# Optimization experiments

Measured on AMD Instinct MI355X. Metric: run time of the kernel, lower is better.

Reference implementation:

```python
import jax, jax.numpy as jnp
import numpy as np
from jax import lax

KERNEL = 512

def squash(x, axis=-1):
    sn = jnp.sum(x * x, axis=axis, keepdims=True)
    scale = sn / (1.0 + sn)
    return scale * x / jnp.sqrt(sn + 1e-8)

def setup_inputs() -> dict:
    key = jax.random.key(0)
    ks = jax.random.split(key, 6)
    x = jax.random.normal(ks[0], (4096, 1, 1008), dtype=jnp.float32)
    a = jax.random.uniform(ks[1], (128, 1, 1), dtype=jnp.float32) * 5.0 + 0.1
    w = jax.random.uniform(ks[2], (128, 1, 1), dtype=jnp.float32) * 150.0 + 1.0
    conv_w = jax.random.normal(ks[3], (256, 128, 16), dtype=jnp.float32) * 0.02
    conv_b = jnp.zeros((256,), dtype=jnp.float32)
    W_caps = jax.random.normal(ks[4], (288, 4, 16, 8), dtype=jnp.float32) * 0.01
    return {"x": x, "a": a, "w": w, "conv_w": conv_w, "conv_b": conv_b, "W_caps": W_caps}

def reference(x, a, w, conv_w, conv_b, W_caps):
    # --- WavConv1d: generate wavelet weights on the fly ---
    t = jnp.linspace(-1.0, 1.0, KERNEL, dtype=jnp.float32).reshape(1, 1, KERNEL)
    a_safe = jnp.clip(a, 1e-5, None)
    t_scaled = t / a_safe
    wav_w = jnp.cos(w * t) * jnp.exp(-0.5 * t_scaled ** 2)  # [128,1,512]
    h = lax.conv_general_dilated(x, wav_w, window_strides=(16,), padding='VALID',
                                 dimension_numbers=('NCH', 'OIH', 'NCH'))  # [B,128,32]
    # --- PrimaryCaps1d ---
    p = lax.conv_general_dilated(h, conv_w, window_strides=(2,), padding='VALID',
                                 dimension_numbers=('NCH', 'OIH', 'NCH'))  # [B,256,9]
    p = p + conv_b[None, :, None]
    B = p.shape[0]
    u = squash(p.reshape(B, -1, 8))  # [B,288,8]
    # --- ClassCaps with dynamic routing ---
    # u_hat[b,c,d,o] = sum_i W_caps[c,d,o,i] * u[b,c,i]
    u_hat = jnp.einsum('cdoi,bci->bcdo', W_caps, u)  # [B,288,4,16]
    b_ij = jnp.zeros((B, u_hat.shape[1], u_hat.shape[2], 1), dtype=u_hat.dtype)
    num_routing = 3
    for i in range(num_routing):
        c_ij = jax.nn.softmax(b_ij, axis=2)                      # [B,288,4,1]
        s_j = jnp.sum(c_ij * u_hat, axis=1, keepdims=True)       # [B,1,4,16]
        v_j = squash(s_j, axis=-1)                               # [B,1,4,16]
        if i < num_routing - 1:
            agreement = jnp.sum(u_hat * v_j, axis=-1, keepdims=True)
            b_ij = b_ij + agreement
    v = jnp.squeeze(v_j, axis=1)          # [B,4,16]
    probs = jnp.linalg.norm(v, axis=-1)   # [B,4]
    return probs, jnp.squeeze(c_ij, axis=-1)  # [B,4], [B,288,4]
```

## Files before the change

### kernel.cpp

```cpp
#include <hip/hip_runtime.h>
#include <hip/hip_bf16.h>
#include <math.h>

typedef __attribute__((ext_vector_type(4))) short short4v;
typedef __attribute__((ext_vector_type(8))) short short8;
typedef __attribute__((ext_vector_type(4))) float f32x4;
typedef __attribute__((ext_vector_type(2))) float f32x2;
typedef _Float16 half8 __attribute__((ext_vector_type(8)));

#define BATCH   4096
#define XLEN    1008
#define NOC1    128
#define NPOS    32
#define NOC2    256
#define NQ      9
#define NCAPS   288
#define NDIM    8

#define BWH_OFF   0
#define BPH_OFF   131072
#define H2_OFF    1179648
#define U_OFF     34734080

static __device__ __forceinline__ short f2h(float v) {
    _Float16 h = (_Float16)v;
    return *reinterpret_cast<short*>(&h);
}

static __device__ __forceinline__ f32x2 pkfma(float a, f32x2 b, f32x2 c) {
    f32x2 av = {a, a};
    return av * b + c;
}

template <int CTRL>
static __device__ __forceinline__ float dpp_addf(float x) {
    int y = __builtin_amdgcn_update_dpp(0, __builtin_bit_cast(int, x),
                                        CTRL, 0xf, 0xf, true);
    return x + __builtin_bit_cast(float, y);
}
static __device__ __forceinline__ float rowsum16(float x) {
    x = dpp_addf<0xB1>(x);
    x = dpp_addf<0x4E>(x);
    x = dpp_addf<0x141>(x);
    x = dpp_addf<0x140>(x);
    return x;
}

__global__ __launch_bounds__(256) void k_pack(const float* __restrict__ a,
                                              const float* __restrict__ w,
                                              const float* __restrict__ cw,
                                              short* __restrict__ bwh,
                                              short* __restrict__ bph) {
    int bid = blockIdx.x;
    int tid = threadIdx.x;
    if (bid < 256) {
        int idx = bid * 256 + tid;
        int e    = idx & 7;
        int lane = (idx >> 3) & 63;
        int s    = (idx >> 9) & 15;
        int nt   = idx >> 13;
        int oc = nt * 16 + (lane & 15);
        int k  = s * 32 + (lane >> 4) * 8 + e;
        float t  = -1.0f + 2.0f * (float)k / 511.0f;
        float av = fmaxf(a[oc], 1e-5f);
        float ts = t / av;
        bwh[idx] = f2h(cosf(w[oc] * t) * expf(-0.5f * ts * ts));
    } else {
        int o = (bid - 256) * 256 + tid;
        int e    = o & 7;
        int lane = (o >> 3) & 63;
        int s    = (o >> 9) & 63;
        int nt   = o >> 15;
        int n  = nt * 16 + (lane & 15);
        int j  = lane >> 4;
        int kk = s >> 2;
        int ic = (s & 3) * 32 + j * 8 + e;
        bph[o] = f2h(cw[(n * NOC1 + ic) * 16 + kk]);
    }
}

__global__ __launch_bounds__(256, 2) void k_wavconv_mfma(
        const float* __restrict__ x,
        const short* __restrict__ bwh,
        short* __restrict__ h2) {
    __shared__ short xl[8][1512];

    int tid = threadIdx.x;
    int b0  = blockIdx.x * 8;

    for (int i4 = tid; i4 < 2016; i4 += 256) {
        int b  = i4 / 252;
        int e4 = i4 - b * 252;
        float4 v = *(const float4*)(x + (size_t)(b0 + b) * XLEN + e4 * 4);
        int i    = e4 * 4;
        int slot = i + 8 * (i >> 4);
        short4v hv;
        hv.x = f2h(v.x); hv.y = f2h(v.y); hv.z = f2h(v.z); hv.w = f2h(v.w);
        *(short4v*)&xl[b][slot] = hv;
    }
    __syncthreads();

    int lane = tid & 63;
    int w    = tid >> 6;
    int col  = lane & 15;
    int rg   = lane >> 4;

    f32x4 acc[4][8];
    f32x4 z = {0.f, 0.f, 0.f, 0.f};
#pragma unroll
    for (int tl = 0; tl < 4; ++tl)
#pragma unroll
        for (int nt = 0; nt < 8; ++nt) acc[tl][nt] = z;

    for (int s = 0; s < 16; ++s) {
        half8 Bh[8];
#pragma unroll
        for (int nt = 0; nt < 8; ++nt) {
            size_t off = ((size_t)(nt * 16 + s) * 64 + lane) * 8;
            Bh[nt] = __builtin_bit_cast(half8, *(const short8*)(bwh + off));
        }
#pragma unroll
        for (int tl = 0; tl < 4; ++tl) {
            int mt  = 4 * w + tl;
            int bl  = mt >> 1;
            int pos = (mt & 1) * 16 + col;
            int i    = (pos + 2 * s) * 16 + rg * 8;
            int slot = i + 8 * (i >> 4);
            half8 ah = __builtin_bit_cast(half8, *(const short8*)&xl[bl][slot]);
#pragma unroll
            for (int nt = 0; nt < 8; ++nt)
                acc[tl][nt] = __builtin_amdgcn_mfma_f32_16x16x32_f16(ah, Bh[nt], acc[tl][nt], 0, 0, 0);
        }
    }

#pragma unroll
    for (int tl = 0; tl < 4; ++tl) {
        int mt = 4 * w + tl;
        int b  = b0 + (mt >> 1);
        int ph = (mt & 1) * 16;
#pragma unroll
        for (int nt = 0; nt < 8; ++nt) {
            int oc = nt * 16 + col;
#pragma unroll
            for (int r = 0; r < 4; ++r) {
                int pos = ph + rg * 4 + r;
                h2[((size_t)b * NPOS + pos) * NOC1 + oc] = f2h(acc[tl][nt][r]);
            }
        }
    }
}

__global__ __launch_bounds__(512, 4) void k_conv_mfma(const short* __restrict__ h2,
                                                      const short* __restrict__ bph,
                                                      const float* __restrict__ cb,
                                                      float* __restrict__ u) {
    __shared__ char smem[36864];
    short* A0 = (short*)smem;
    short* A1 = (short*)(smem + 6400);
    float* p_lds = (float*)smem;

    int tid  = threadIdx.x;
    int w    = tid >> 6;
    int lane = tid & 63;
    int col  = lane & 15;
    int rg   = lane >> 4;
    int b0   = blockIdx.x * 8;

    f32x4 acc[5][2];
    f32x4 z = {0.f, 0.f, 0.f, 0.f};
#pragma unroll
    for (int mt = 0; mt < 5; ++mt) { acc[mt][0] = z; acc[mt][1] = z; }

    auto stageA = [&](int s, short* dst) {
        int kk  = s >> 2;
        int icb = (s & 3) * 32;
        if (tid < 288) {
            int m = tid >> 2;
            int g = tid & 3;
            const short* src = h2 +
                ((size_t)(b0 + (m & 7)) * NPOS + (2 * (m >> 3) + kk)) * NOC1 + icb + g * 8;
            *(short8*)&dst[m * 40 + g * 8] = *(const short8*)src;
        }
    };

    auto mfmaStep = [&](int s, const short* A) {
        short8 arow[5];
#pragma unroll
        for (int mt = 0; mt < 5; ++mt)
            arow[mt] = *(const short8*)&A[(mt * 16 + col) * 40 + rg * 8];
#pragma unroll
        for (int n = 0; n < 2; ++n) {
            size_t bo = ((size_t)((w + n * 8) * 64 + s) * 64 + lane) * 8;
            half8 Bh = __builtin_bit_cast(half8, *(const short8*)(bph + bo));
#pragma unroll
            for (int mt = 0; mt < 5; ++mt)
                acc[mt][n] = __builtin_amdgcn_mfma_f32_16x16x32_f16(
                    __builtin_bit_cast(half8, arow[mt]), Bh, acc[mt][n], 0, 0, 0);
        }
    };

    stageA(0, A0);
    __syncthreads();
    for (int s = 0; s < 64; s += 2) {
        if (s + 1 < 64) stageA(s + 1, A1);
        mfmaStep(s, A0);
        __syncthreads();
        if (s + 2 < 64) stageA(s + 2, A0);
        mfmaStep(s + 1, A1);
        __syncthreads();
    }

    int oc2l = w * 16 + col;
    for (int n = 0; n < 2; ++n) {
        float bias = cb[n * 128 + oc2l];
#pragma unroll
        for (int mt = 0; mt < 5; ++mt)
#pragma unroll
            for (int r = 0; r < 4; ++r) {
                int m = mt * 16 + rg * 4 + r;
                if (m < 72)
                    p_lds[(m & 7) * 1152 + oc2l * 9 + (m >> 3)] = acc[mt][n][r] + bias;
            }
        __syncthreads();
        for (int idx = tid; idx < 1152; idx += 512) {
            int lb = idx / 144;
            int cl = idx - lb * 144;
            float* ppt = &p_lds[lb * 1152 + cl * 8];
            float sn = 0.f;
#pragma unroll
            for (int i = 0; i < NDIM; ++i) sn = fmaf(ppt[i], ppt[i], sn);
            float sc = sn / (1.f + sn) / sqrtf(sn + 1e-8f);
            float* ug = u + ((size_t)(b0 + lb) * (NCAPS * NDIM) + (n * 144 + cl) * 8);
            float4 u0 = make_float4(ppt[0] * sc, ppt[1] * sc, ppt[2] * sc, ppt[3] * sc);
            float4 u1 = make_float4(ppt[4] * sc, ppt[5] * sc, ppt[6] * sc, ppt[7] * sc);
            ((float4*)ug)[0] = u0;
            ((float4*)ug)[1] = u1;
        }
        __syncthreads();
    }
}

__global__ __launch_bounds__(512, 4) void k_routing(const float* __restrict__ u,
                                                    const float* __restrict__ Wc,
                                                    float* __restrict__ out) {
    __shared__ float b_lds[2][NCAPS * 4];
    __shared__ float c_lds[2][NCAPS * 4];
    __shared__ float part_lds[2][512];
    __shared__ float v_lds[2][64];

    int tid = threadIdx.x;
    int b0  = blockIdx.x * 2;

    int g = tid >> 6;
    int l = tid & 63;
    int d = l >> 4;
    int o = l & 15;
    int gu = __builtin_amdgcn_readfirstlane(g);

    const float* ub0 = u + (size_t)(b0 + 0) * (NCAPS * NDIM) + gu * 36 * NDIM;
    const float* ub1 = u + (size_t)(b0 + 1) * (NCAPS * NDIM) + gu * 36 * NDIM;

    f32x2 uh[36];
#pragma unroll
    for (int c = 0; c < 36; ++c) {
        int cap = gu * 36 + c;
        const float4* W4 = (const float4*)(Wc + ((size_t)cap * 512) + l * 8);
        float4 A  = W4[0];
        float4 Bv = W4[1];
        f32x2 u0 = {ub0[c * 8 + 0], ub1[c * 8 + 0]};
        f32x2 u1 = {ub0[c * 8 + 1], ub1[c * 8 + 1]};
        f32x2 u2 = {ub0[c * 8 + 2], ub1[c * 8 + 2]};
        f32x2 u3 = {ub0[c * 8 + 3], ub1[c * 8 + 3]};
        f32x2 u4 = {ub0[c * 8 + 4], ub1[c * 8 + 4]};
        f32x2 u5 = {ub0[c * 8 + 5], ub1[c * 8 + 5]};
        f32x2 u6 = {ub0[c * 8 + 6], ub1[c * 8 + 6]};
        f32x2 u7 = {ub0[c * 8 + 7], ub1[c * 8 + 7]};
        f32x2 t = (f32x2){A.x, A.x} * u0;
        t = pkfma(A.y,  u1, t);
        t = pkfma(A.z,  u2, t);
        t = pkfma(A.w,  u3, t);
        t = pkfma(Bv.x, u4, t);
        t = pkfma(Bv.y, u5, t);
        t = pkfma(Bv.z, u6, t);
        t = pkfma(Bv.w, u7, t);
        uh[c] = t;
    }

    for (int r = 0; r < 3; ++r) {
        if (r > 0) {
            __builtin_amdgcn_wave_barrier();
            for (int i = l; i < 72; i += 64) {
                int bb = (i >= 36) ? 1 : 0;
                int cl = i - bb * 36;
                int c  = gu * 36 + cl;
                float4 bv = *(const float4*)&b_lds[bb][c * 4];
                float m  = fmaxf(fmaxf(bv.x, bv.y), fmaxf(bv.z, bv.w));
                float e0 = expf(bv.x - m), e1 = expf(bv.y - m);
                float e2 = expf(bv.z - m), e3 = expf(bv.w - m);
                float inv = 1.f / (e0 + e1 + e2 + e3);
                e0 *= inv; e1 *= inv; e2 *= inv; e3 *= inv;
                *(float4*)&c_lds[bb][c * 4] = make_float4(e0, e1, e2, e3);
                if (r == 2) {
                    *(float4*)(out + 16384 + ((size_t)(b0 + bb) * NCAPS + c) * 4) =
                        make_float4(e0, e1, e2, e3);
                }
            }
            __builtin_amdgcn_wave_barrier();
        }

        f32x2 p = {0.f, 0.f};
        if (r == 0) {
#pragma unroll
            for (int c = 0; c < 36; ++c)
                p = pkfma(0.25f, uh[c], p);
        } else {
#pragma unroll
            for (int c = 0; c < 36; ++c) {
                f32x2 c2 = {c_lds[0][(g * 36 + c) * 4 + d],
                            c_lds[1][(g * 36 + c) * 4 + d]};
                p = c2 * uh[c] + p;
            }
        }
        part_lds[0][tid] = p.x;
        part_lds[1][tid] = p.y;
        __syncthreads();

        if (tid < 128) {
            int bb = tid >> 6;
            int ll = tid & 63;
            float sv = 0.f;
#pragma unroll
            for (int k = 0; k < 8; ++k) sv += part_lds[bb][ll + 64 * k];
            float sq = rowsum16(sv * sv);
            float sc = sq / (1.f + sq) / sqrtf(sq + 1e-8f);
            float v  = sv * sc;
            v_lds[bb][ll] = v;
            if (r == 2) {
                float vv = rowsum16(v * v);
                if ((ll & 15) == 0)
                    out[(size_t)(b0 + bb) * 4 + (ll >> 4)] = sqrtf(vv);
            }
        }
        __syncthreads();

        if (r < 2) {
            f32x2 v01 = {v_lds[0][l], v_lds[1][l]};
#pragma unroll
            for (int c = 0; c < 36; ++c) {
                f32x2 t2 = uh[c] * v01;
                float t0 = rowsum16(t2.x);
                float t1 = rowsum16(t2.y);
                if (o == 0) {
                    if (r == 0) {
                        b_lds[0][(g * 36 + c) * 4 + d] = t0;
                        b_lds[1][(g * 36 + c) * 4 + d] = t1;
                    } else {
                        b_lds[0][(g * 36 + c) * 4 + d] += t0;
                        b_lds[1][(g * 36 + c) * 4 + d] += t1;
                    }
                }
            }
        }
    }
}

extern "C" void kernel_launch(void* const* d_in, const int* in_sizes, int n_in,
                              void* d_out, int out_size, void* d_ws, size_t ws_size,
                              hipStream_t stream) {
    const float* x      = (const float*)d_in[0];
    const float* a      = (const float*)d_in[1];
    const float* w      = (const float*)d_in[2];
    const float* conv_w = (const float*)d_in[3];
    const float* conv_b = (const float*)d_in[4];
    const float* W_caps = (const float*)d_in[5];
    float* out = (float*)d_out;
    char* ws   = (char*)d_ws;

    short*  bwh = (short*)(ws + BWH_OFF);
    short*  bph = (short*)(ws + BPH_OFF);
    short*  h2  = (short*)(ws + H2_OFF);
    float*  u   = (float*)(ws + U_OFF);

    k_pack<<<2304, 256, 0, stream>>>(a, w, conv_w, bwh, bph);
    k_wavconv_mfma<<<BATCH / 8, 256, 0, stream>>>(x, bwh, h2);
    k_conv_mfma<<<BATCH / 8, 512, 0, stream>>>(h2, bph, conv_b, u);
    k_routing<<<BATCH / 2, 512, 0, stream>>>(u, W_caps, out);
}
```

Before: 238.1 us.

## Process four batch items per routing block with 16 waves and 18 capsules each

The routing kernel now runs 1024-thread blocks that each handle four batch items instead of two. Each wave owns 18 capsules instead of 36 and keeps predictions for two item pairs in registers. Every W_caps load is therefore reused across four items, and each thread does half as many capsule iterations per item pair. In exchange the blocks are larger, the cross-wave reduction doubles to 16 partials, and the LDS footprint grows, which may reduce occupancy.

```diff
diff --git a/kernel.cpp b/kernel.cpp
--- a/kernel.cpp
+++ b/kernel.cpp
@@ -240,16 +240,16 @@
     }
 }
 
-__global__ __launch_bounds__(512, 4) void k_routing(const float* __restrict__ u,
-                                                    const float* __restrict__ Wc,
-                                                    float* __restrict__ out) {
-    __shared__ float b_lds[2][NCAPS * 4];
-    __shared__ float c_lds[2][NCAPS * 4];
-    __shared__ float part_lds[2][512];
-    __shared__ float v_lds[2][64];
+__global__ __launch_bounds__(1024, 4) void k_routing(const float* __restrict__ u,
+                                                     const float* __restrict__ Wc,
+                                                     float* __restrict__ out) {
+    __shared__ float b_lds[4][NCAPS * 4];
+    __shared__ float c_lds[4][NCAPS * 4];
+    __shared__ float part_lds[4][1024];
+    __shared__ float v_lds[4][64];
 
     int tid = threadIdx.x;
-    int b0  = blockIdx.x * 2;
+    int b0  = blockIdx.x * 4;
 
     int g = tid >> 6;
     int l = tid & 63;
@@ -257,42 +257,45 @@
     int o = l & 15;
     int gu = __builtin_amdgcn_readfirstlane(g);
 
-    const float* ub0 = u + (size_t)(b0 + 0) * (NCAPS * NDIM) + gu * 36 * NDIM;
-    const float* ub1 = u + (size_t)(b0 + 1) * (NCAPS * NDIM) + gu * 36 * NDIM;
-
-    f32x2 uh[36];
-#pragma unroll
-    for (int c = 0; c < 36; ++c) {
-        int cap = gu * 36 + c;
+    const float* ub0 = u + (size_t)(b0 + 0) * (NCAPS * NDIM) + gu * 18 * NDIM;
+    const float* ub1 = u + (size_t)(b0 + 1) * (NCAPS * NDIM) + gu * 18 * NDIM;
+    const float* ub2 = u + (size_t)(b0 + 2) * (NCAPS * NDIM) + gu * 18 * NDIM;
+    const float* ub3 = u + (size_t)(b0 + 3) * (NCAPS * NDIM) + gu * 18 * NDIM;
+
+    f32x2 uhA[18], uhB[18];
+#pragma unroll
+    for (int c = 0; c < 18; ++c) {
+        int cap = gu * 18 + c;
         const float4* W4 = (const float4*)(Wc + ((size_t)cap * 512) + l * 8);
         float4 A  = W4[0];
         float4 Bv = W4[1];
-        f32x2 u0 = {ub0[c * 8 + 0], ub1[c * 8 + 0]};
-        f32x2 u1 = {ub0[c * 8 + 1], ub1[c * 8 + 1]};
-        f32x2 u2 = {ub0[c * 8 + 2], ub1[c * 8 + 2]};
-        f32x2 u3 = {ub0[c * 8 + 3], ub1[c * 8 + 3]};
-        f32x2 u4 = {ub0[c * 8 + 4], ub1[c * 8 + 4]};
-        f32x2 u5 = {ub0[c * 8 + 5], ub1[c * 8 + 5]};
-        f32x2 u6 = {ub0[c * 8 + 6], ub1[c * 8 + 6]};
-        f32x2 u7 = {ub0[c * 8 + 7], ub1[c * 8 + 7]};
-        f32x2 t = (f32x2){A.x, A.x} * u0;
-        t = pkfma(A.y,  u1, t);
-        t = pkfma(A.z,  u2, t);
-        t = pkfma(A.w,  u3, t);
-        t = pkfma(Bv.x, u4, t);
-        t = pkfma(Bv.y, u5, t);
-        t = pkfma(Bv.z, u6, t);
-        t = pkfma(Bv.w, u7, t);
-        uh[c] = t;
+        f32x2 tA = (f32x2){A.x, A.x} * (f32x2){ub0[c * 8 + 0], ub1[c * 8 + 0]};
+        tA = pkfma(A.y,  (f32x2){ub0[c * 8 + 1], ub1[c * 8 + 1]}, tA);
+        tA = pkfma(A.z,  (f32x2){ub0[c * 8 + 2], ub1[c * 8 + 2]}, tA);
+        tA = pkfma(A.w,  (f32x2){ub0[c * 8 + 3], ub1[c * 8 + 3]}, tA);
+        tA = pkfma(Bv.x, (f32x2){ub0[c * 8 + 4], ub1[c * 8 + 4]}, tA);
+        tA = pkfma(Bv.y, (f32x2){ub0[c * 8 + 5], ub1[c * 8 + 5]}, tA);
+        tA = pkfma(Bv.z, (f32x2){ub0[c * 8 + 6], ub1[c * 8 + 6]}, tA);
+        tA = pkfma(Bv.w, (f32x2){ub0[c * 8 + 7], ub1[c * 8 + 7]}, tA);
+        uhA[c] = tA;
+        f32x2 tB = (f32x2){A.x, A.x} * (f32x2){ub2[c * 8 + 0], ub3[c * 8 + 0]};
+        tB = pkfma(A.y,  (f32x2){ub2[c * 8 + 1], ub3[c * 8 + 1]}, tB);
+        tB = pkfma(A.z,  (f32x2){ub2[c * 8 + 2], ub3[c * 8 + 2]}, tB);
+        tB = pkfma(A.w,  (f32x2){ub2[c * 8 + 3], ub3[c * 8 + 3]}, tB);
+        tB = pkfma(Bv.x, (f32x2){ub2[c * 8 + 4], ub3[c * 8 + 4]}, tB);
+        tB = pkfma(Bv.y, (f32x2){ub2[c * 8 + 5], ub3[c * 8 + 5]}, tB);
+        tB = pkfma(Bv.z, (f32x2){ub2[c * 8 + 6], ub3[c * 8 + 6]}, tB);
+        tB = pkfma(Bv.w, (f32x2){ub2[c * 8 + 7], ub3[c * 8 + 7]}, tB);
+        uhB[c] = tB;
     }
 
     for (int r = 0; r < 3; ++r) {
         if (r > 0) {
             __builtin_amdgcn_wave_barrier();
             for (int i = l; i < 72; i += 64) {
-                int bb = (i >= 36) ? 1 : 0;
-                int cl = i - bb * 36;
-                int c  = gu * 36 + cl;
+                int bb = i / 18;
+                int cl = i - bb * 18;
+                int c  = gu * 18 + cl;
                 float4 bv = *(const float4*)&b_lds[bb][c * 4];
                 float m  = fmaxf(fmaxf(bv.x, bv.y), fmaxf(bv.z, bv.w));
                 float e0 = expf(bv.x - m), e1 = expf(bv.y - m);
@@ -308,29 +311,35 @@
             __builtin_amdgcn_wave_barrier();
         }
 
-        f32x2 p = {0.f, 0.f};
+        f32x2 pA = {0.f, 0.f}, pB = {0.f, 0.f};
         if (r == 0) {
 #pragma unroll
-            for (int c = 0; c < 36; ++c)
-                p = pkfma(0.25f, uh[c], p);
+            for (int c = 0; c < 18; ++c) {
+                pA = pkfma(0.25f, uhA[c], pA);
+                pB = pkfma(0.25f, uhB[c], pB);
+            }
         } else {
 #pragma unroll
-            for (int c = 0; c < 36; ++c) {
-                f32x2 c2 = {c_lds[0][(g * 36 + c) * 4 + d],
-                            c_lds[1][(g * 36 + c) * 4 + d]};
-                p = c2 * uh[c] + p;
-            }
-        }
-        part_lds[0][tid] = p.x;
-        part_lds[1][tid] = p.y;
-        __syncthreads();
-
-        if (tid < 128) {
+            for (int c = 0; c < 18; ++c) {
+                int idx4 = (gu * 18 + c) * 4 + d;
+                f32x2 cA = {c_lds[0][idx4], c_lds[1][idx4]};
+                f32x2 cB = {c_lds[2][idx4], c_lds[3][idx4]};
+                pA = cA * uhA[c] + pA;
+                pB = cB * uhB[c] + pB;
+            }
+        }
+        part_lds[0][tid] = pA.x;
+        part_lds[1][tid] = pA.y;
+        part_lds[2][tid] = pB.x;
+        part_lds[3][tid] = pB.y;
+        __syncthreads();
+
+        if (tid < 256) {
             int bb = tid >> 6;
             int ll = tid & 63;
             float sv = 0.f;
 #pragma unroll
-            for (int k = 0; k < 8; ++k) sv += part_lds[bb][ll + 64 * k];
+            for (int k = 0; k < 16; ++k) sv += part_lds[bb][ll + 64 * k];
             float sq = rowsum16(sv * sv);
             float sc = sq / (1.f + sq) / sqrtf(sq + 1e-8f);
             float v  = sv * sc;
@@ -344,19 +353,28 @@
         __syncthreads();
 
         if (r < 2) {
-            f32x2 v01 = {v_lds[0][l], v_lds[1][l]};
-#pragma unroll
-            for (int c = 0; c < 36; ++c) {
-                f32x2 t2 = uh[c] * v01;
-                float t0 = rowsum16(t2.x);
-                float t1 = rowsum16(t2.y);
+            f32x2 vA = {v_lds[0][l], v_lds[1][l]};
+            f32x2 vB = {v_lds[2][l], v_lds[3][l]};
+#pragma unroll
+            for (int c = 0; c < 18; ++c) {
+                f32x2 tA = uhA[c] * vA;
+                f32x2 tB = uhB[c] * vB;
+                float t0 = rowsum16(tA.x);
+                float t1 = rowsum16(tA.y);
+                float t2 = rowsum16(tB.x);
+                float t3 = rowsum16(tB.y);
                 if (o == 0) {
+                    int idx4 = (gu * 18 + c) * 4 + d;
                     if (r == 0) {
-                        b_lds[0][(g * 36 + c) * 4 + d] = t0;
-                        b_lds[1][(g * 36 + c) * 4 + d] = t1;
+                        b_lds[0][idx4] = t0;
+                        b_lds[1][idx4] = t1;
+                        b_lds[2][idx4] = t2;
+                        b_lds[3][idx4] = t3;
                     } else {
-                        b_lds[0][(g * 36 + c) * 4 + d] += t0;
-                        b_lds[1][(g * 36 + c) * 4 + d] += t1;
+                        b_lds[0][idx4] += t0;
+                        b_lds[1][idx4] += t1;
+                        b_lds[2][idx4] += t2;
+                        b_lds[3][idx4] += t3;
                     }
                 }
             }
@@ -384,5 +402,5 @@
     k_pack<<<2304, 256, 0, stream>>>(a, w, conv_w, bwh, bph);
     k_wavconv_mfma<<<BATCH / 8, 256, 0, stream>>>(x, bwh, h2);
     k_conv_mfma<<<BATCH / 8, 512, 0, stream>>>(h2, bph, conv_b, u);
-    k_routing<<<BATCH / 2, 512, 0, stream>>>(u, W_caps, out);
-}
+    k_routing<<<BATCH / 4, 1024, 0, stream>>>(u, W_caps, out);
+}
```

Measured after the change: 245.3 us. +3.0%, slower.
